# Optimization experiments

Measured on AMD Instinct MI355X. Metric: run time of the kernel, lower is better.

## Reference

```python
import jax, jax.numpy as jnp
import numpy as np

B, L, D = 2, 2048, 1024
H, G = 16, 2            # num_heads, num_kv_groups
HPG = H // G            # heads per kv group = 8
DQK, DV = 128, 128      # qk_head_dim, v_head_dim (head_dim=64, ratios=2.0)


def setup_inputs() -> dict:
    key = jax.random.key(0)
    ks = jax.random.split(key, 12)

    def xavier(k, shape, scale=1.0):
        fan_in, fan_out = shape[0], shape[1]
        lim = np.sqrt(6.0 / (fan_in + fan_out))
        return jax.random.uniform(k, shape, jnp.float32, -lim, lim) * scale

    return {
        "in_q": jax.random.normal(ks[0], (B, L, D), jnp.float32),
        "in_k": jax.random.normal(ks[1], (B, L, D), jnp.float32),
        "in_v": jax.random.normal(ks[2], (B, L, D), jnp.float32),
        # weights stored as [in, out] (transpose of torch Linear); qk_init_scale=0.5
        "Wq": xavier(ks[3], (D, H * DQK), 0.5),
        "bq": jnp.zeros((H * DQK,), jnp.float32),
        "Wk": xavier(ks[4], (D, G * DQK), 0.5),
        "bk": jnp.zeros((G * DQK,), jnp.float32),
        "Wv": xavier(ks[5], (D, G * DV)),
        "bv": jnp.zeros((G * DV,), jnp.float32),
        "Wo": xavier(ks[6], (H * DV, D)),
        "bo": jnp.zeros((D,), jnp.float32),
        "q_extra_scale": jnp.ones((1,), jnp.float32),
    }


def reference(in_q, in_k, in_v, Wq, bq, Wk, bk, Wv, bv, Wo, bo, q_extra_scale):
    # fused projections
    q = (in_q @ Wq + bq) * q_extra_scale              # [B,L,H*DQK]
    k = in_k @ Wk + bk                                 # [B,L,G*DQK]
    v = in_v @ Wv + bv                                 # [B,L,G*DV]

    # reshape: keep GQA group structure instead of materializing repeat_interleave
    q = q.reshape(B, L, G, HPG, DQK)                   # heads grouped: head h = g*HPG + m
    k = k.reshape(B, L, G, DQK)
    v = v.reshape(B, L, G, DV)

    scale = 1.0 / np.sqrt(DQK)
    # scores: [B,G,HPG,L_q,L_kv]
    scores = jnp.einsum("bsgmd,btgd->bgmst", q, k) * scale
    causal = jnp.tril(jnp.ones((L, L), bool))          # is_causal=True
    scores = jnp.where(causal, scores, jnp.finfo(scores.dtype).min)
    attn = jax.nn.softmax(scores, axis=-1)
    ctx = jnp.einsum("bgmst,btgd->bsgmd", attn, v)     # [B,L,G,HPG,DV]
    ctx = ctx.reshape(B, L, H * DV)
    return ctx @ Wo + bo                               # [B,L,D]
```

## Files before the change

### kernel.cpp

```cpp
#include <hip/hip_runtime.h>


typedef __bf16 bf16;
typedef __bf16 bf16x8 __attribute__((ext_vector_type(8)));
typedef __bf16 bf16x4 __attribute__((ext_vector_type(4)));
typedef float f32x4 __attribute__((ext_vector_type(4)));
typedef float f32x16 __attribute__((ext_vector_type(16)));
typedef float float4v __attribute__((ext_vector_type(4)));

#define MFMA_BF16(a, b, c) __builtin_amdgcn_mfma_f32_16x16x32_bf16((a), (b), (c), 0, 0, 0)
#define MFMA32(a, b, c)    __builtin_amdgcn_mfma_f32_32x32x16_bf16((a), (b), (c), 0, 0, 0)

static constexpr int Bz = 2, Lz = 2048, Dz = 1024;
static constexpr int Hz = 16, Gz = 2;
static constexpr int DQKz = 128, DVz = 128;

__device__ __forceinline__ void async_copy16(const bf16* g, bf16* l) {
    __builtin_amdgcn_global_load_lds(
        (const __attribute__((address_space(1))) unsigned int*)g,
        (__attribute__((address_space(3))) unsigned int*)l, 16, 0, 0);
}

__global__ __launch_bounds__(256) void prep(
    const float* __restrict__ q, const float* __restrict__ k,
    const float* __restrict__ v, bf16* __restrict__ dq,
    bf16* __restrict__ dk, bf16* __restrict__ dv,
    const float* __restrict__ Wq, const float* __restrict__ Wk,
    const float* __restrict__ Wv, const float* __restrict__ Wo,
    bf16* __restrict__ WqT, bf16* __restrict__ WkT,
    bf16* __restrict__ WvT, bf16* __restrict__ WoT)
{
    int bid = blockIdx.x;
    if (bid < 6144) {
        const float* s = bid < 2048 ? q : (bid < 4096 ? k : v);
        bf16* d = bid < 2048 ? dq : (bid < 4096 ? dk : dv);
        int i = (bid & 2047) * 2048 + threadIdx.x * 8;
        float4v a = *(const float4v*)(s + i);
        float4v b = *(const float4v*)(s + i + 4);
        bf16x8 o;
        #pragma unroll
        for (int j = 0; j < 4; ++j) { o[j] = (bf16)a[j]; o[j + 4] = (bf16)b[j]; }
        *(bf16x8*)(d + i) = o;
        return;
    }
    bid -= 6144;
    const float* W; bf16* WT; int K, N;
    if (bid < 2048)      { W = Wq; WT = WqT; K = 1024; N = 2048; }
    else if (bid < 2304) { W = Wk; WT = WkT; K = 1024; N = 256;  bid -= 2048; }
    else if (bid < 2560) { W = Wv; WT = WvT; K = 1024; N = 256;  bid -= 2304; }
    else                 { W = Wo; WT = WoT; K = 2048; N = 1024; bid -= 2560; }
    int tiles_n = N >> 5;
    int n0 = (bid % tiles_n) * 32, k0 = (bid / tiles_n) * 32;

    __shared__ bf16 t[32][33];
    int tx = threadIdx.x & 31, ty = threadIdx.x >> 5;
    #pragma unroll
    for (int i = 0; i < 4; ++i)
        t[ty + i * 8][tx] = (bf16)W[(size_t)(k0 + ty + i * 8) * N + n0 + tx];
    __syncthreads();
    #pragma unroll
    for (int i = 0; i < 4; ++i)
        WT[(size_t)(n0 + ty + i * 8) * K + k0 + tx] = t[tx][ty + i * 8];
}

template <typename TC>
__device__ __forceinline__ void gemm_tile4(
    const bf16* __restrict__ A, const bf16* __restrict__ BT,
    const float* __restrict__ bias, float scale, TC* __restrict__ C,
    int M, int N, int K, int m0, int n0, bool trans_out,
    bf16 (&As)[2][128 * 64], bf16 (&Bs)[2][128 * 64])
{
    const int tid  = threadIdx.x;
    const int wave = tid >> 6;
    const int lane = tid & 63;
    const int quad = lane >> 4;
    const int l16  = lane & 15;
    const int sw   = l16 & 7;
    const int wm = wave >> 1, wn = wave & 1;

    f32x4 acc[4][4] = {};

    auto stage = [&](int k0, int buf) {
        #pragma unroll
        for (int s = 0; s < 4; ++s) {
            int i = s * 256 + tid;
            int row = i >> 3, c = (i & 7) ^ (row & 7);
            async_copy16(A + (size_t)(m0 + row) * K + k0 + c * 8, &As[buf][i * 8]);
        }
        #pragma unroll
        for (int s = 0; s < 4; ++s) {
            int i = s * 256 + tid;
            int row = i >> 3, c = (i & 7) ^ (row & 7);
            async_copy16(BT + (size_t)(n0 + row) * K + k0 + c * 8, &Bs[buf][i * 8]);
        }
    };

    stage(0, 0);
    int cur = 0;
    for (int k0 = 0; k0 < K; k0 += 64) {
        __syncthreads();
        if (k0 + 64 < K) stage(k0 + 64, cur ^ 1);

        #pragma unroll
        for (int ks = 0; ks < 2; ++ks) {
            bf16x8 af[4], bfv[4];
            #pragma unroll
            for (int mt = 0; mt < 4; ++mt)
                af[mt] = *(const bf16x8*)(&As[cur][((wm * 64 + mt * 16 + l16) * 8
                                                    + ((ks * 4 + quad) ^ sw)) * 8]);
            #pragma unroll
            for (int nt = 0; nt < 4; ++nt)
                bfv[nt] = *(const bf16x8*)(&Bs[cur][((wn * 64 + nt * 16 + l16) * 8
                                                     + ((ks * 4 + quad) ^ sw)) * 8]);
            #pragma unroll
            for (int mt = 0; mt < 4; ++mt)
                #pragma unroll
                for (int nt = 0; nt < 4; ++nt)
                    acc[mt][nt] = MFMA_BF16(af[mt], bfv[nt], acc[mt][nt]);
        }
        cur ^= 1;
    }

    #pragma unroll
    for (int nt = 0; nt < 4; ++nt) {
        int col = n0 + wn * 64 + nt * 16 + l16;
        float bv = bias[col];
        #pragma unroll
        for (int mt = 0; mt < 4; ++mt) {
            int row = m0 + wm * 64 + mt * 16 + quad * 4;
            if (trans_out) {
                struct V4 { TC v[4]; } o;
                #pragma unroll
                for (int r = 0; r < 4; ++r)
                    o.v[r] = (TC)((acc[mt][nt][r] + bv) * scale);
                *(V4*)(&C[(size_t)col * M + row]) = o;
            } else {
                #pragma unroll
                for (int r = 0; r < 4; ++r)
                    C[(size_t)(row + r) * N + col] =
                        (TC)((acc[mt][nt][r] + bv) * scale);
            }
        }
    }
}

__global__ __launch_bounds__(256, 2) void proj_qkv(
    const bf16* __restrict__ aq, const bf16* __restrict__ ak,
    const bf16* __restrict__ av, const bf16* __restrict__ WqT,
    const bf16* __restrict__ WkT, const bf16* __restrict__ WvT,
    const float* __restrict__ bq, const float* __restrict__ bk,
    const float* __restrict__ bv, const float* __restrict__ qsc,
    bf16* __restrict__ Qw, bf16* __restrict__ Kw, bf16* __restrict__ VwT)
{
    __shared__ bf16 As[2][128 * 64];
    __shared__ bf16 Bs[2][128 * 64];
    int bid = blockIdx.x;
    if (bid < 512) {
        int xcd = bid & 7, rest = bid >> 3;
        int n = rest & 15, mg = rest >> 4;
        int m = mg * 8 + xcd;
        float scale = qsc[0] * 0.08838834764831845f * 1.4426950408889634f;
        gemm_tile4<bf16>(aq, WqT, bq, scale, Qw, 4096, 2048, 1024,
                         m * 128, n * 128, false, As, Bs);
    } else if (bid < 576) {
        int b2 = bid - 512;
        gemm_tile4<bf16>(ak, WkT, bk, 1.0f, Kw, 4096, 256, 1024,
                         (b2 >> 1) * 128, (b2 & 1) * 128, false, As, Bs);
    } else {
        int b2 = bid - 576;
        gemm_tile4<bf16>(av, WvT, bv, 1.0f, VwT, 4096, 256, 1024,
                         (b2 >> 1) * 128, (b2 & 1) * 128, true, As, Bs);
    }
}

__global__ __launch_bounds__(256, 3) void proj_o(
    const bf16* __restrict__ Cw, const bf16* __restrict__ WoT,
    const float* __restrict__ bo, float* __restrict__ out)
{
    __shared__ bf16 As[2][128 * 64];
    __shared__ bf16 Bs[2][64 * 64];

    const int tid  = threadIdx.x;
    const int wave = tid >> 6;
    const int lane = tid & 63;
    const int quad = lane >> 4;
    const int l16  = lane & 15;
    const int sw   = l16 & 7;
    const int wm = wave >> 1, wn = wave & 1;

    int xcd = blockIdx.x & 7, rest = blockIdx.x >> 3;
    int n = rest & 15, mg = rest >> 4;
    int m = mg * 8 + xcd;
    const int m0 = m * 128, n0 = n * 64;
    const int M = 4096, N = 1024, K = 2048;

    f32x4 acc[4][2] = {};

    auto stage = [&](int k0, int buf) {
        #pragma unroll
        for (int s = 0; s < 4; ++s) {
            int i = s * 256 + tid;
            int row = i >> 3, c = (i & 7) ^ (row & 7);
            async_copy16(Cw + (size_t)(m0 + row) * K + k0 + c * 8, &As[buf][i * 8]);
        }
        #pragma unroll
        for (int s = 0; s < 2; ++s) {
            int i = s * 256 + tid;
            int row = i >> 3, c = (i & 7) ^ (row & 7);
            async_copy16(WoT + (size_t)(n0 + row) * K + k0 + c * 8, &Bs[buf][i * 8]);
        }
    };

    stage(0, 0);
    int cur = 0;
    for (int k0 = 0; k0 < K; k0 += 64) {
        __syncthreads();
        if (k0 + 64 < K) stage(k0 + 64, cur ^ 1);

        #pragma unroll
        for (int ks = 0; ks < 2; ++ks) {
            bf16x8 af[4], bfv[2];
            #pragma unroll
            for (int mt = 0; mt < 4; ++mt)
                af[mt] = *(const bf16x8*)(&As[cur][((wm * 64 + mt * 16 + l16) * 8
                                                    + ((ks * 4 + quad) ^ sw)) * 8]);
            #pragma unroll
            for (int nt = 0; nt < 2; ++nt)
                bfv[nt] = *(const bf16x8*)(&Bs[cur][((wn * 32 + nt * 16 + l16) * 8
                                                     + ((ks * 4 + quad) ^ sw)) * 8]);
            #pragma unroll
            for (int mt = 0; mt < 4; ++mt)
                #pragma unroll
                for (int nt = 0; nt < 2; ++nt)
                    acc[mt][nt] = MFMA_BF16(af[mt], bfv[nt], acc[mt][nt]);
        }
        cur ^= 1;
    }

    #pragma unroll
    for (int nt = 0; nt < 2; ++nt) {
        int col = n0 + wn * 32 + nt * 16 + l16;
        float bv = bo[col];
        #pragma unroll
        for (int mt = 0; mt < 4; ++mt) {
            int row = m0 + wm * 64 + mt * 16 + quad * 4;
            #pragma unroll
            for (int r = 0; r < 4; ++r)
                out[(size_t)(row + r) * N + col] = acc[mt][nt][r] + bv;
        }
    }
}

__global__ __launch_bounds__(256, 2) void attn_fused(
    const bf16* __restrict__ Q,
    const bf16* __restrict__ Kp,
    const bf16* __restrict__ VT,
    bf16* __restrict__ ctx)
{
    __shared__ bf16 Kb[2][64 * 128];
    __shared__ bf16 Vb[2][128 * 64];
    __shared__ bf16 Ps[4][32 * 64];

    const int tid  = threadIdx.x;
    const int wave = tid >> 6;
    const int lane = tid & 63;
    const int l32  = lane & 31;
    const int half = lane >> 5;
    const int sw8  = lane & 7;

    const int bid = blockIdx.x;
    const int hg  = bid >> 8;
    const int rem = bid & 255;
    const int hq  = (rem & 7) >> 1;
    const int b   = rem & 1;
    const int p   = rem >> 3;
    const int qt  = hg ? p : (63 - p);

    const int g = hq >> 1;
    const int h = hq * 4 + wave;

    const int q0   = qt * 32;
    const int nkt  = (qt >> 1) + 1;
    const int qrow = q0 + l32;

    const bf16* kgbase = Kp + (size_t)(b * Lz) * (Gz * DQKz) + g * DQKz;
    const bf16* vgbase = VT + (size_t)(g * DVz) * (Bz * Lz) + b * Lz;

    auto stage = [&](int kt, int buf) {
        const bf16* kb = kgbase + (size_t)(kt * 64) * (Gz * DQKz);
        #pragma unroll
        for (int s = 0; s < 4; ++s) {
            int i = s * 256 + tid;
            int key = i >> 4, c = (i & 15) ^ (key & 7);
            async_copy16(kb + (size_t)key * (Gz * DQKz) + c * 8, &Kb[buf][i * 8]);
        }
        const bf16* vb = vgbase + kt * 64;
        #pragma unroll
        for (int s = 0; s < 4; ++s) {
            int i = s * 256 + tid;
            int dv = i >> 3, c = (i & 7) ^ (dv & 7);
            async_copy16(vb + (size_t)dv * (Bz * Lz) + c * 8, &Vb[buf][i * 8]);
        }
    };

    bf16x8 qf[8];
    {
        const bf16* qbase = Q + (size_t)(b * Lz + qrow) * (Hz * DQKz) + h * DQKz;
        #pragma unroll
        for (int kc = 0; kc < 8; ++kc)
            qf[kc] = *(const bf16x8*)(qbase + kc * 16 + half * 8);
    }

    bf16* ps = Ps[wave];
    f32x16 oacc[4] = {};
    float lsum = 0.0f;

    stage(0, 0);
    int cur = 0;

    for (int kt = 0; kt < nkt; ++kt) {
        __syncthreads();
        if (kt + 1 < nkt) stage(kt + 1, cur ^ 1);

        const bf16* kcur = Kb[cur];
        const bf16* vcur = Vb[cur];

        f32x16 sacc[2] = {};
        #pragma unroll
        for (int kg = 0; kg < 2; ++kg) {
            const int row = kg * 32 + l32;
            #pragma unroll
            for (int kc = 0; kc < 8; ++kc) {
                bf16x8 kf = *(const bf16x8*)(&kcur[row * 128
                                                   + (((kc * 2 + half) ^ sw8) * 8)]);
                sacc[kg] = MFMA32(kf, qf[kc], sacc[kg]);
            }
        }

        const int kv0 = kt * 64;
        const bool diag = (kt == nkt - 1);
        #pragma unroll
        for (int kg = 0; kg < 2; ++kg) {
            float pv[16];
            if (diag) {
                #pragma unroll
                for (int r = 0; r < 16; ++r) {
                    int key = kv0 + kg * 32 + (r & 3) + 8 * (r >> 2) + 4 * half;
                    pv[r] = (key > qrow) ? 0.0f : exp2f(sacc[kg][r]);
                }
            } else {
                #pragma unroll
                for (int r = 0; r < 16; ++r)
                    pv[r] = exp2f(sacc[kg][r]);
            }
            #pragma unroll
            for (int r = 0; r < 16; ++r) lsum += pv[r];
            #pragma unroll
            for (int i = 0; i < 4; ++i) {
                bf16x4 pk;
                #pragma unroll
                for (int r = 0; r < 4; ++r) pk[r] = (bf16)pv[i * 4 + r];
                int chunk = i + kg * 4;
                *(bf16x4*)(&ps[l32 * 64 + ((chunk ^ sw8) << 3) + half * 4]) = pk;
            }
        }

        #pragma unroll
        for (int kc = 0; kc < 4; ++kc) {
            bf16x8 pf = *(const bf16x8*)(&ps[l32 * 64
                                             + (((kc * 2 + half) ^ sw8) << 3)]);
            #pragma unroll
            for (int dvg = 0; dvg < 4; ++dvg) {
                const int row = dvg * 32 + l32;
                bf16x8 vf = *(const bf16x8*)(&vcur[row * 64
                                                   + (((kc * 2 + half) ^ sw8) * 8)]);
                oacc[dvg] = MFMA32(vf, pf, oacc[dvg]);
            }
        }
        cur ^= 1;
    }

    lsum += __shfl_xor(lsum, 32);
    const float inv = 1.0f / lsum;

    bf16* cb = ctx + (size_t)(b * Lz + qrow) * (Hz * DVz) + h * DVz;
    #pragma unroll
    for (int dvg = 0; dvg < 4; ++dvg) {
        #pragma unroll
        for (int i = 0; i < 4; ++i) {
            bf16x4 o4;
            #pragma unroll
            for (int r = 0; r < 4; ++r)
                o4[r] = (bf16)(oacc[dvg][i * 4 + r] * inv);
            *(bf16x4*)(&cb[dvg * 32 + 8 * i + 4 * half]) = o4;
        }
    }
}

extern "C" void kernel_launch(void* const* d_in, const int* in_sizes, int n_in,
                              void* d_out, int out_size, void* d_ws, size_t ws_size,
                              hipStream_t stream)
{
    (void)in_sizes; (void)n_in; (void)out_size; (void)ws_size;

    const float* in_q = (const float*)d_in[0];
    const float* in_k = (const float*)d_in[1];
    const float* in_v = (const float*)d_in[2];
    const float* Wq   = (const float*)d_in[3];
    const float* bq   = (const float*)d_in[4];
    const float* Wk   = (const float*)d_in[5];
    const float* bk   = (const float*)d_in[6];
    const float* Wv   = (const float*)d_in[7];
    const float* bv   = (const float*)d_in[8];
    const float* Wo   = (const float*)d_in[9];
    const float* bo   = (const float*)d_in[10];
    const float* qsc  = (const float*)d_in[11];
    float* out = (float*)d_out;

    const int M = Bz * Lz;

    bf16* aq  = (bf16*)d_ws;
    bf16* WqT = aq  + (size_t)M * Dz;
    bf16* WkT = WqT + (size_t)2048 * 1024;
    bf16* WvT = WkT + (size_t)256 * 1024;
    bf16* WoT = WvT + (size_t)256 * 1024;
    bf16* Qw  = WoT + (size_t)1024 * 2048;
    bf16* Kw  = Qw  + (size_t)M * 2048;
    bf16* VwT = Kw  + (size_t)M * 256;
    bf16* Cw  = VwT + (size_t)256 * M;
    bf16* ak  = Cw;
    bf16* av  = Cw + (size_t)M * Dz;

    prep<<<dim3(10752), dim3(256), 0, stream>>>(
        in_q, in_k, in_v, aq, ak, av, Wq, Wk, Wv, Wo, WqT, WkT, WvT, WoT);

    proj_qkv<<<dim3(640), dim3(256), 0, stream>>>(
        aq, ak, av, WqT, WkT, WvT, bq, bk, bv, qsc, Qw, Kw, VwT);

    attn_fused<<<dim3(512), dim3(256), 0, stream>>>(Qw, Kw, VwT, Cw);

    proj_o<<<dim3(512), dim3(256), 0, stream>>>(Cw, WoT, bo, out);
}
```

Before: 258.3 us.

## Split KV tile across wave pairs and pair causal q-tiles per block

Each block now handles two heads, with two waves per head each taking half of every 64-key tile. Partial outputs and row sums are reduced through LDS at the end, reusing the K/V buffers as scratch. Each block also processes a long and a short causal query tile in sequence to balance work. The per-wave register and P-buffer footprint shrinks, but fewer heads share each staged K/V tile and there is an extra cross-wave reduction with barriers.

```diff
diff --git a/kernel.cpp b/kernel.cpp
--- a/kernel.cpp
+++ b/kernel.cpp
@@ -259,7 +259,8 @@
 {
     __shared__ bf16 Kb[2][64 * 128];
     __shared__ bf16 Vb[2][128 * 64];
-    __shared__ bf16 Ps[4][32 * 64];
+    __shared__ bf16 Ps[4][32 * 32];
+    __shared__ float Ls[4 * 32];
 
     const int tid  = threadIdx.x;
     const int wave = tid >> 6;
@@ -269,19 +270,12 @@
     const int sw8  = lane & 7;
 
     const int bid = blockIdx.x;
-    const int hg  = bid >> 8;
-    const int rem = bid & 255;
-    const int hq  = (rem & 7) >> 1;
-    const int b   = rem & 1;
-    const int p   = rem >> 3;
-    const int qt  = hg ? p : (63 - p);
-
-    const int g = hq >> 1;
-    const int h = hq * 4 + wave;
-
-    const int q0   = qt * 32;
-    const int nkt  = (qt >> 1) + 1;
-    const int qrow = q0 + l32;
+    const int b   = bid & 1;
+    const int g   = (bid >> 1) & 1;
+    const int hp  = (bid >> 2) & 3;
+    const int p   = bid >> 4;
+    const int h   = g * 8 + hp * 2 + (wave & 1);
+    const int kg  = wave >> 1;
 
     const bf16* kgbase = Kp + (size_t)(b * Lz) * (Gz * DQKz) + g * DQKz;
     const bf16* vgbase = VT + (size_t)(g * DVz) * (Bz * Lz) + b * Lz;
@@ -303,96 +297,129 @@
         }
     };
 
-    bf16x8 qf[8];
-    {
-        const bf16* qbase = Q + (size_t)(b * Lz + qrow) * (Hz * DQKz) + h * DQKz;
-        #pragma unroll
-        for (int kc = 0; kc < 8; ++kc)
-            qf[kc] = *(const bf16x8*)(qbase + kc * 16 + half * 8);
-    }
-
     bf16* ps = Ps[wave];
-    f32x16 oacc[4] = {};
-    float lsum = 0.0f;
-
-    stage(0, 0);
-    int cur = 0;
-
-    for (int kt = 0; kt < nkt; ++kt) {
-        __syncthreads();
-        if (kt + 1 < nkt) stage(kt + 1, cur ^ 1);
-
-        const bf16* kcur = Kb[cur];
-        const bf16* vcur = Vb[cur];
-
-        f32x16 sacc[2] = {};
-        #pragma unroll
-        for (int kg = 0; kg < 2; ++kg) {
-            const int row = kg * 32 + l32;
-            #pragma unroll
-            for (int kc = 0; kc < 8; ++kc) {
-                bf16x8 kf = *(const bf16x8*)(&kcur[row * 128
-                                                   + (((kc * 2 + half) ^ sw8) * 8)]);
-                sacc[kg] = MFMA32(kf, qf[kc], sacc[kg]);
-            }
-        }
-
-        const int kv0 = kt * 64;
-        const bool diag = (kt == nkt - 1);
-        #pragma unroll
-        for (int kg = 0; kg < 2; ++kg) {
+
+    for (int pass = 0; pass < 2; ++pass) {
+        const int qt   = pass == 0 ? (63 - p) : p;
+        const int q0   = qt * 32;
+        const int nkt  = (qt >> 1) + 1;
+        const int qrow = q0 + l32;
+
+        bf16x8 qf[8];
+        {
+            const bf16* qbase = Q + (size_t)(b * Lz + qrow) * (Hz * DQKz) + h * DQKz;
+            #pragma unroll
+            for (int kc = 0; kc < 8; ++kc)
+                qf[kc] = *(const bf16x8*)(qbase + kc * 16 + half * 8);
+        }
+
+        f32x16 oacc[4] = {};
+        float lsum = 0.0f;
+
+        if (pass) __syncthreads();
+        stage(0, 0);
+        int cur = 0;
+
+        for (int kt = 0; kt < nkt; ++kt) {
+            __syncthreads();
+            if (kt + 1 < nkt) stage(kt + 1, cur ^ 1);
+
+            const bf16* kcur = Kb[cur];
+            const bf16* vcur = Vb[cur];
+
+            f32x16 sacc = {};
+            {
+                const int row = kg * 32 + l32;
+                #pragma unroll
+                for (int kc = 0; kc < 8; ++kc) {
+                    bf16x8 kf = *(const bf16x8*)(&kcur[row * 128
+                                                       + (((kc * 2 + half) ^ sw8) * 8)]);
+                    sacc = MFMA32(kf, qf[kc], sacc);
+                }
+            }
+
+            const int kv0 = kt * 64;
             float pv[16];
-            if (diag) {
+            if (kt == nkt - 1) {
                 #pragma unroll
                 for (int r = 0; r < 16; ++r) {
                     int key = kv0 + kg * 32 + (r & 3) + 8 * (r >> 2) + 4 * half;
-                    pv[r] = (key > qrow) ? 0.0f : exp2f(sacc[kg][r]);
+                    pv[r] = (key > qrow) ? 0.0f : exp2f(sacc[r]);
                 }
             } else {
                 #pragma unroll
                 for (int r = 0; r < 16; ++r)
-                    pv[r] = exp2f(sacc[kg][r]);
+                    pv[r] = exp2f(sacc[r]);
             }
             #pragma unroll
             for (int r = 0; r < 16; ++r) lsum += pv[r];
+
             #pragma unroll
             for (int i = 0; i < 4; ++i) {
                 bf16x4 pk;
                 #pragma unroll
                 for (int r = 0; r < 4; ++r) pk[r] = (bf16)pv[i * 4 + r];
-                int chunk = i + kg * 4;
-                *(bf16x4*)(&ps[l32 * 64 + ((chunk ^ sw8) << 3) + half * 4]) = pk;
-            }
-        }
-
-        #pragma unroll
-        for (int kc = 0; kc < 4; ++kc) {
-            bf16x8 pf = *(const bf16x8*)(&ps[l32 * 64
-                                             + (((kc * 2 + half) ^ sw8) << 3)]);
+                *(bf16x4*)(&ps[l32 * 32 + 8 * i + 4 * half]) = pk;
+            }
+
+            #pragma unroll
+            for (int kc = 0; kc < 2; ++kc) {
+                bf16x8 pf = *(const bf16x8*)(&ps[l32 * 32 + kc * 16 + half * 8]);
+                #pragma unroll
+                for (int dvg = 0; dvg < 4; ++dvg) {
+                    const int row = dvg * 32 + l32;
+                    int chunk = kg * 4 + kc * 2 + half;
+                    bf16x8 vf = *(const bf16x8*)(&vcur[row * 64
+                                                       + ((chunk ^ sw8) * 8)]);
+                    oacc[dvg] = MFMA32(vf, pf, oacc[dvg]);
+                }
+            }
+            cur ^= 1;
+        }
+
+        lsum += __shfl_xor(lsum, 32);
+
+        __syncthreads();
+        if (kg == 1) {
+            float* sc = (wave == 2) ? (float*)&Kb[0][0] : (float*)&Vb[0][0];
             #pragma unroll
             for (int dvg = 0; dvg < 4; ++dvg) {
-                const int row = dvg * 32 + l32;
-                bf16x8 vf = *(const bf16x8*)(&vcur[row * 64
-                                                   + (((kc * 2 + half) ^ sw8) * 8)]);
-                oacc[dvg] = MFMA32(vf, pf, oacc[dvg]);
-            }
-        }
-        cur ^= 1;
-    }
-
-    lsum += __shfl_xor(lsum, 32);
-    const float inv = 1.0f / lsum;
-
-    bf16* cb = ctx + (size_t)(b * Lz + qrow) * (Hz * DVz) + h * DVz;
-    #pragma unroll
-    for (int dvg = 0; dvg < 4; ++dvg) {
-        #pragma unroll
-        for (int i = 0; i < 4; ++i) {
-            bf16x4 o4;
-            #pragma unroll
-            for (int r = 0; r < 4; ++r)
-                o4[r] = (bf16)(oacc[dvg][i * 4 + r] * inv);
-            *(bf16x4*)(&cb[dvg * 32 + 8 * i + 4 * half]) = o4;
+                #pragma unroll
+                for (int i = 0; i < 4; ++i) {
+                    float4v o4;
+                    #pragma unroll
+                    for (int r = 0; r < 4; ++r) o4[r] = oacc[dvg][i * 4 + r];
+                    *(float4v*)(&sc[lane * 68 + dvg * 16 + i * 4]) = o4;
+                }
+            }
+            if (half == 0) Ls[wave * 32 + l32] = lsum;
+        }
+        __syncthreads();
+        if (kg == 0) {
+            float* sc = (wave == 0) ? (float*)&Kb[0][0] : (float*)&Vb[0][0];
+            #pragma unroll
+            for (int dvg = 0; dvg < 4; ++dvg) {
+                #pragma unroll
+                for (int i = 0; i < 4; ++i) {
+                    float4v o4 = *(const float4v*)(&sc[lane * 68 + dvg * 16 + i * 4]);
+                    #pragma unroll
+                    for (int r = 0; r < 4; ++r) oacc[dvg][i * 4 + r] += o4[r];
+                }
+            }
+            const float inv = 1.0f / (lsum + Ls[(wave + 2) * 32 + l32]);
+
+            bf16* cb = ctx + (size_t)(b * Lz + qrow) * (Hz * DVz) + h * DVz;
+            #pragma unroll
+            for (int dvg = 0; dvg < 4; ++dvg) {
+                #pragma unroll
+                for (int i = 0; i < 4; ++i) {
+                    bf16x4 o4;
+                    #pragma unroll
+                    for (int r = 0; r < 4; ++r)
+                        o4[r] = (bf16)(oacc[dvg][i * 4 + r] * inv);
+                    *(bf16x4*)(&cb[dvg * 32 + 8 * i + 4 * half]) = o4;
+                }
+            }
         }
     }
 }
```

Result: no change. 260.0 us (+0.7%).
